# Kernel optimization log

Hardware: AMD Instinct MI355X
Metric: run time of the kernel (lower is better)

The kernel has to match this reference:

```python
import jax, jax.numpy as jnp
import numpy as np

MU = jnp.array([1.0, 0.9, 0.7, 0.5, 0.3, 0.1, -0.1, -0.3, -0.5, -0.7, -0.9], dtype=jnp.float32)
SIGMA = jnp.array([1e-3] + [0.1] * 10, dtype=jnp.float32)
H = 8  # n_head


def _lin(x, W, b):
    return x @ W.T + b


def _knrm_logsum(eq, ed, mq, md):
    # eq:[B,Q,D] ed:[B,L,D] mq:[B,Q] md:[B,L] -> [B,K]
    qn = eq / jnp.maximum(jnp.linalg.norm(eq, axis=2, keepdims=True), 1e-12)
    dn = ed / jnp.maximum(jnp.linalg.norm(ed, axis=2, keepdims=True), 1e-12)
    sim = jnp.einsum('bqe,bde->bqd', qn, dn)
    pv = jnp.exp(-(sim[..., None] - MU) ** 2 / (2.0 * SIGMA ** 2))  # [B,Q,L,K]
    ps = jnp.sum(pv * md[:, None, :, None], axis=2)                 # [B,Q,K]
    lps = jnp.log(jnp.clip(ps, 1e-10, None)) * mq[..., None] * 0.01
    return jnp.sum(lps, axis=1)


def _mha(x, Wq, bq, Wk, bk, Wv, bv, Wo, bo):
    # CyberZHG-style MultiHeadAttention: relu on q/k/v projections and output.
    B, L, D = x.shape
    dh = D // H

    def split(t):
        return t.reshape(B, L, H, dh).transpose(0, 2, 1, 3)

    q = split(jax.nn.relu(_lin(x, Wq, bq)))
    k = split(jax.nn.relu(_lin(x, Wk, bk)))
    v = split(jax.nn.relu(_lin(x, Wv, bv)))
    att = jax.nn.softmax(jnp.einsum('bhqe,bhke->bhqk', q, k) / jnp.sqrt(jnp.float32(dh)), axis=-1)
    y = jnp.einsum('bhqk,bhke->bhqe', att, v).transpose(0, 2, 1, 3).reshape(B, L, D)
    return jax.nn.relu(_lin(y, Wo, bo))


def _forward(masks_q, masks_d, masks_dcq, masks_dbody, emb, Wq, bq, Wk, bk, Wv, bv, Wo, bo,
             tW, tb, qdW, qdb, qbW, qbb, qcqW, qcqb, dcqW, dcqb, bcqW, bcqb,
             expW, expb, combW, combb, inputs_q, inputs_d, inputs_dcq, inputs_dbody):
    eq = emb[inputs_q]
    ed = emb[inputs_d]
    eb = emb[inputs_dbody]
    qd = jnp.tanh(_lin(_knrm_logsum(eq, ed, masks_q, masks_d), qdW, qdb))
    qb = jnp.tanh(_lin(_knrm_logsum(eq, eb, masks_q, masks_dbody), qbW, qbb))
    B, MN, ML = inputs_dcq.shape
    e_dcq = jax.nn.relu(_lin(emb[inputs_dcq.reshape(B, MN * ML)], tW, tb))
    enc_dcq = _mha(e_dcq, Wq, bq, Wk, bk, Wv, bv, Wo, bo).reshape(B, MN, ML, -1)
    enc_d = _mha(ed, Wq, bq, Wk, bk, Wv, bv, Wo, bo)
    enc_b = _mha(eb, Wq, bq, Wk, bk, Wv, bv, Wo, bo)

    def per_cq(i_dcq, m_dcq):  # i_dcq:[B,ML,D] m_dcq:[B,ML]
        return (_knrm_logsum(eq, i_dcq, masks_q, m_dcq),
                _knrm_logsum(enc_d, i_dcq, masks_d, m_dcq),
                _knrm_logsum(enc_b, i_dcq, masks_dbody, m_dcq))

    kq, kd, kb = jax.vmap(per_cq, in_axes=(1, 1))(enc_dcq, masks_dcq)  # [MN,B,K]
    qcqres = jnp.tanh(_lin(kq, qcqW, qcqb))      # [MN,B,1]
    qcqdattn = jnp.tanh(_lin(kd, dcqW, dcqb))
    qcqbattn = jnp.tanh(_lin(kb, bcqW, bcqb))
    qcqd = jnp.sum(qcqres * qcqdattn, axis=0)    # [B,1]
    qcqb2 = jnp.sum(qcqres * qcqbattn, axis=0)
    qcq = _lin(jnp.concatenate([qcqd, qcqb2], axis=1), expW, expb)
    return jnp.tanh(_lin(jnp.concatenate([qd, qb, qcq], axis=1), combW, combb)).squeeze()


def setup_inputs():
    B, Q, DL, BL, MN, ML, D, V = 32, 20, 64, 512, 8, 16, 128, 50000
    key = jax.random.key(0)
    ks = jax.random.split(key, 40)

    def w(i, shape, s=0.05):
        return jax.random.normal(ks[i], shape, jnp.float32) * s

    return {
        'inputs_q': jax.random.randint(ks[0], (B, Q), 1, V),
        'inputs_d': jax.random.randint(ks[1], (B, DL), 1, V),
        'inputs_dcq': jax.random.randint(ks[2], (B, MN, ML), 1, V),
        'inputs_dbody': jax.random.randint(ks[3], (B, BL), 1, V),
        'masks_q': jnp.ones((B, Q), jnp.float32),
        'masks_d': jnp.ones((B, DL), jnp.float32),
        'masks_dcq': jnp.ones((B, MN, ML), jnp.float32),
        'masks_dbody': jnp.ones((B, BL), jnp.float32),
        'emb': w(4, (V, D), 0.1).at[0].set(0.0),  # padding_idx=0
        'Wq': w(5, (D, D)), 'bq': w(6, (D,)),
        'Wk': w(7, (D, D)), 'bk': w(8, (D,)),
        'Wv': w(9, (D, D)), 'bv': w(10, (D,)),
        'Wo': w(11, (D, D)), 'bo': w(12, (D,)),
        'tW': w(13, (D, D)), 'tb': w(14, (D,)),
        'qdW': w(15, (1, 11)), 'qdb': w(16, (1,)),
        'qbW': w(17, (1, 11)), 'qbb': w(18, (1,)),
        'qcqW': w(19, (1, 11)), 'qcqb': w(20, (1,)),
        'dcqW': w(21, (1, 11)), 'dcqb': w(22, (1,)),
        'bcqW': w(23, (1, 11)), 'bcqb': w(24, (1,)),
        'expW': w(25, (1, 2)), 'expb': w(26, (1,)),
        'combW': w(27, (1, 3)), 'combb': w(28, (1,)),
    }


def reference(inputs_q, inputs_d, inputs_dcq, inputs_dbody, masks_q, masks_d, masks_dcq, masks_dbody,
              emb, Wq, bq, Wk, bk, Wv, bv, Wo, bo, tW, tb, qdW, qdb, qbW, qbb, qcqW, qcqb,
              dcqW, dcqb, bcqW, bcqb, expW, expb, combW, combb):
    return _forward(masks_q, masks_d, masks_dcq, masks_dbody, emb, Wq, bq, Wk, bk, Wv, bv, Wo, bo,
                    tW, tb, qdW, qdb, qbW, qbb, qcqW, qcqb, dcqW, dcqb, bcqW, bcqb,
                    expW, expb, combW, combb, inputs_q, inputs_d, inputs_dcq, inputs_dbody)
```

## Files before the change

kernel.cpp:

```cpp
#include <hip/hip_runtime.h>
#include <hip/hip_bf16.h>

#define BB 32
#define QL_ 20
#define DL_ 64
#define BL_ 512
#define MN_ 8
#define ML_ 16
#define DD 128
#define HH 8

#define ROWS_DCQ 4096
#define ROWS_D   2048
#define ROWS_B   16384
#define R_ALL    22528
#define ROWS_EQ  640
#define R_GATHER 23168

typedef float f2 __attribute__((ext_vector_type(2)));

__global__ __launch_bounds__(256) void gather_all(
    const int* __restrict__ in_q, const int* __restrict__ in_d,
    const int* __restrict__ in_dcq, const int* __restrict__ in_db,
    const float* __restrict__ emb, float* __restrict__ x_all, float* __restrict__ ytmp,
    float* __restrict__ inv_eq, float* __restrict__ inv_ed, float* __restrict__ inv_eb,
    float* __restrict__ zero_p, int nzero) {
    int blk = blockIdx.x;
    if (blk >= 2896) {
        int i = (blk - 2896) * 256 + threadIdx.x;
        if (i < nzero) zero_p[i] = 0.f;
        return;
    }
    int t = blk * 256 + threadIdx.x;
    int r = t >> 5, c = t & 31;
    const int* idx; float* outp; float* invp; int lr;
    if (r < ROWS_DCQ)              { idx = in_dcq; outp = ytmp + (size_t)r * DD;  invp = nullptr; lr = r; }
    else if (r < ROWS_DCQ + ROWS_D){ idx = in_d;   outp = x_all + (size_t)r * DD; invp = inv_ed;  lr = r - ROWS_DCQ; }
    else if (r < R_ALL)            { idx = in_db;  outp = x_all + (size_t)r * DD; invp = inv_eb;  lr = r - (ROWS_DCQ + ROWS_D); }
    else                           { idx = in_q;   outp = x_all + (size_t)r * DD; invp = inv_eq;  lr = r - R_ALL; }
    float4 val = ((const float4*)(emb + (size_t)idx[lr] * DD))[c];
    ((float4*)outp)[c] = val;
    float ss = val.x * val.x + val.y * val.y + val.z * val.z + val.w * val.w;
    ss += __shfl_xor(ss, 1, 64);
    ss += __shfl_xor(ss, 2, 64);
    ss += __shfl_xor(ss, 4, 64);
    ss += __shfl_xor(ss, 8, 64);
    ss += __shfl_xor(ss, 16, 64);
    if (c == 0 && invp) invp[lr] = 1.0f / fmaxf(sqrtf(ss), 1e-12f);
}

__device__ __forceinline__ void linear_body(float* __restrict__ wT, float* __restrict__ bs,
                                            const float* __restrict__ in, const float* __restrict__ W,
                                            const float* __restrict__ bias, float* __restrict__ out,
                                            float* __restrict__ inv_out, int block) {
    int t = threadIdx.x;
    for (int i = t; i < DD * DD; i += 256) {
        int o = i >> 7, e = i & 127;
        wT[e * 132 + o] = W[i];
    }
    if (t < 128) bs[t] = bias[t];
    __syncthreads();
    int og = t & 15, rg = t >> 4;
    int rowbase = block * 128 + rg * 8;
    f2 acc[8][4];
#pragma unroll
    for (int r = 0; r < 8; r++)
#pragma unroll
        for (int p = 0; p < 4; p++) acc[r][p] = f2{0.f, 0.f};
    for (int e4 = 0; e4 < 32; e4++) {
        float4 xv[8];
#pragma unroll
        for (int r = 0; r < 8; r++)
            xv[r] = *(const float4*)&in[(size_t)(rowbase + r) * DD + 4 * e4];
#pragma unroll
        for (int ee = 0; ee < 4; ee++) {
            int e = 4 * e4 + ee;
            float4 wa = *(const float4*)&wT[e * 132 + 8 * og];
            float4 wb = *(const float4*)&wT[e * 132 + 8 * og + 4];
            f2 w0 = {wa.x, wa.y}, w1 = {wa.z, wa.w}, w2 = {wb.x, wb.y}, w3 = {wb.z, wb.w};
#pragma unroll
            for (int r = 0; r < 8; r++) {
                float x = ((const float*)&xv[r])[ee];
                f2 x2 = {x, x};
                acc[r][0] = __builtin_elementwise_fma(x2, w0, acc[r][0]);
                acc[r][1] = __builtin_elementwise_fma(x2, w1, acc[r][1]);
                acc[r][2] = __builtin_elementwise_fma(x2, w2, acc[r][2]);
                acc[r][3] = __builtin_elementwise_fma(x2, w3, acc[r][3]);
            }
        }
    }
    float4 ba = *(const float4*)&bs[8 * og];
    float4 bbv = *(const float4*)&bs[8 * og + 4];
    float ss[8];
#pragma unroll
    for (int r = 0; r < 8; r++) {
        float o0 = fmaxf(acc[r][0].x + ba.x, 0.f);
        float o1 = fmaxf(acc[r][0].y + ba.y, 0.f);
        float o2 = fmaxf(acc[r][1].x + ba.z, 0.f);
        float o3 = fmaxf(acc[r][1].y + ba.w, 0.f);
        float o4 = fmaxf(acc[r][2].x + bbv.x, 0.f);
        float o5 = fmaxf(acc[r][2].y + bbv.y, 0.f);
        float o6 = fmaxf(acc[r][3].x + bbv.z, 0.f);
        float o7 = fmaxf(acc[r][3].y + bbv.w, 0.f);
        float4 s1 = {o0, o1, o2, o3}, s2 = {o4, o5, o6, o7};
        float* op = out + (size_t)(rowbase + r) * DD + 8 * og;
        *(float4*)op = s1;
        *(float4*)(op + 4) = s2;
        ss[r] = o0 * o0 + o1 * o1 + o2 * o2 + o3 * o3 + o4 * o4 + o5 * o5 + o6 * o6 + o7 * o7;
    }
    if (inv_out) {
#pragma unroll
        for (int r = 0; r < 8; r++) {
            ss[r] += __shfl_xor(ss[r], 1, 64);
            ss[r] += __shfl_xor(ss[r], 2, 64);
            ss[r] += __shfl_xor(ss[r], 4, 64);
            ss[r] += __shfl_xor(ss[r], 8, 64);
        }
#pragma unroll
        for (int r = 0; r < 8; r++)
            if (og == r) inv_out[rowbase + r] = 1.0f / fmaxf(sqrtf(ss[r]), 1e-12f);
    }
}

__global__ __launch_bounds__(256) void lin_kernel(const float* __restrict__ in, const float* __restrict__ W,
                                                  const float* __restrict__ bias, float* __restrict__ out,
                                                  float* __restrict__ inv_out) {
    __shared__ float wT[DD * 132];
    __shared__ float bs[DD];
    linear_body(wT, bs, in, W, bias, out, inv_out, blockIdx.x);
}

__global__ __launch_bounds__(256) void qkv_all(const float* __restrict__ x,
                                               const float* __restrict__ Wq, const float* __restrict__ bq,
                                               const float* __restrict__ Wk, const float* __restrict__ bk,
                                               const float* __restrict__ Wv, const float* __restrict__ bv,
                                               float* __restrict__ q, float* __restrict__ k, float* __restrict__ v) {
    __shared__ float wT[DD * 132];
    __shared__ float bs[DD];
    int sel = blockIdx.x / 176, blk = blockIdx.x % 176;
    const float* W = (sel == 0) ? Wq : (sel == 1) ? Wk : Wv;
    const float* B = (sel == 0) ? bq : (sel == 1) ? bk : bv;
    float* O = (sel == 0) ? q : (sel == 1) ? k : v;
    linear_body(wT, bs, x, W, B, O, nullptr, blk);
}

__device__ __forceinline__ void attn512_v6(float* __restrict__ sm,
                                           const float* __restrict__ q, const float* __restrict__ k,
                                           const float* __restrict__ v, float* __restrict__ y,
                                           int b, int h) {
    float* ks = sm;
    float* vs = sm + 512 * 16;
    int t = threadIdx.x;
    const size_t base = (size_t)b * 512 * DD + h * 16;
    for (int i = t; i < 512 * 4; i += 512) {
        int j = i >> 2, c = i & 3;
        *(float4*)&ks[j * 16 + 4 * c] = *(const float4*)&k[base + (size_t)j * DD + 4 * c];
        *(float4*)&vs[j * 16 + 4 * c] = *(const float4*)&v[base + (size_t)j * DD + 4 * c];
    }
    int w = t >> 6, lane = t & 63;
    int kg = w & 3, qw = w >> 2;
    int r0 = qw * 256 + lane;
    f2 qv[2][16];
#pragma unroll
    for (int p = 0; p < 2; p++) {
        const float* qa = q + base + (size_t)(r0 + p * 128) * DD;
        const float* qb2 = qa + 64 * DD;
#pragma unroll
        for (int c = 0; c < 4; c++) {
            float4 va = *(const float4*)(qa + 4 * c);
            float4 vb = *(const float4*)(qb2 + 4 * c);
            qv[p][4 * c + 0] = f2{va.x * 0.25f, vb.x * 0.25f};
            qv[p][4 * c + 1] = f2{va.y * 0.25f, vb.y * 0.25f};
            qv[p][4 * c + 2] = f2{va.z * 0.25f, vb.z * 0.25f};
            qv[p][4 * c + 3] = f2{va.w * 0.25f, vb.w * 0.25f};
        }
    }
    f2 acc[2][16];
    f2 l2[2] = {f2{0.f, 0.f}, f2{0.f, 0.f}};
#pragma unroll
    for (int p = 0; p < 2; p++)
#pragma unroll
        for (int e = 0; e < 16; e++) acc[p][e] = f2{0.f, 0.f};
    __syncthreads();
    int j0 = kg * 128;
    for (int j = j0; j < j0 + 128; j++) {
        float kk[16], vv[16];
#pragma unroll
        for (int c = 0; c < 4; c++) {
            *(float4*)&kk[4 * c] = *(const float4*)&ks[j * 16 + 4 * c];
            *(float4*)&vv[4 * c] = *(const float4*)&vs[j * 16 + 4 * c];
        }
        f2 d0a = qv[0][0] * f2{kk[0], kk[0]};
        f2 d1a = qv[0][1] * f2{kk[1], kk[1]};
        f2 d0b = qv[1][0] * f2{kk[0], kk[0]};
        f2 d1b = qv[1][1] * f2{kk[1], kk[1]};
#pragma unroll
        for (int e = 2; e < 16; e += 2) {
            d0a = __builtin_elementwise_fma(qv[0][e], f2{kk[e], kk[e]}, d0a);
            d1a = __builtin_elementwise_fma(qv[0][e + 1], f2{kk[e + 1], kk[e + 1]}, d1a);
            d0b = __builtin_elementwise_fma(qv[1][e], f2{kk[e], kk[e]}, d0b);
            d1b = __builtin_elementwise_fma(qv[1][e + 1], f2{kk[e + 1], kk[e + 1]}, d1b);
        }
        f2 da = d0a + d1a, db = d0b + d1b;
        f2 pa = {__expf(da.x), __expf(da.y)};
        f2 pb = {__expf(db.x), __expf(db.y)};
        l2[0] += pa;
        l2[1] += pb;
#pragma unroll
        for (int e = 0; e < 16; e++) {
            f2 ve = {vv[e], vv[e]};
            acc[0][e] = __builtin_elementwise_fma(pa, ve, acc[0][e]);
            acc[1][e] = __builtin_elementwise_fma(pb, ve, acc[1][e]);
        }
    }
    __syncthreads();
#pragma unroll
    for (int g = 1; g < 4; g++) {
        if (kg == g) {
#pragma unroll
            for (int p = 0; p < 2; p++) {
                int ra = r0 + p * 128;
                float* pa = &sm[ra * 20];
                float* pb = &sm[(ra + 64) * 20];
#pragma unroll
                for (int e = 0; e < 16; e++) { pa[e] = acc[p][e].x; pb[e] = acc[p][e].y; }
                pa[16] = l2[p].x;
                pb[16] = l2[p].y;
            }
        }
        __syncthreads();
        if (kg == 0) {
#pragma unroll
            for (int p = 0; p < 2; p++) {
                int ra = r0 + p * 128;
                const float* pa = &sm[ra * 20];
                const float* pb = &sm[(ra + 64) * 20];
#pragma unroll
                for (int e = 0; e < 16; e++) { acc[p][e].x += pa[e]; acc[p][e].y += pb[e]; }
                l2[p].x += pa[16];
                l2[p].y += pb[16];
            }
        }
        __syncthreads();
    }
    if (kg == 0) {
#pragma unroll
        for (int p = 0; p < 2; p++) {
            float ix = 1.0f / l2[p].x, iy = 1.0f / l2[p].y;
            float o0[16], o1[16];
#pragma unroll
            for (int e = 0; e < 16; e++) { o0[e] = acc[p][e].x * ix; o1[e] = acc[p][e].y * iy; }
            float* yp0 = y + base + (size_t)(r0 + p * 128) * DD;
            float* yp1 = yp0 + 64 * DD;
#pragma unroll
            for (int c = 0; c < 4; c++) {
                *(float4*)(yp0 + 4 * c) = *(const float4*)&o0[4 * c];
                *(float4*)(yp1 + 4 * c) = *(const float4*)&o1[4 * c];
            }
        }
    }
}

template <int L, int NQ>
__device__ __forceinline__ void attn_body(float* __restrict__ sm, const float* __restrict__ q,
                                          const float* __restrict__ k, const float* __restrict__ v,
                                          float* __restrict__ y, int b, int h) {
    constexpr int WAVES = 8;
    constexpr int WQ = L / (32 * NQ);
    constexpr int KG = WAVES / WQ;
    constexpr int KPG = L / KG;
    float* ks = sm;
    float* vs = sm + L * 16;
    int t = threadIdx.x;
    const size_t base = (size_t)b * L * DD + h * 16;
    for (int i = t; i < L * 4; i += 512) {
        int j = i >> 2, c = i & 3;
        *(float4*)&ks[j * 16 + 4 * c] = *(const float4*)&k[base + (size_t)j * DD + 4 * c];
        *(float4*)&vs[j * 16 + 4 * c] = *(const float4*)&v[base + (size_t)j * DD + 4 * c];
    }
    int w = t >> 6, lane = t & 63;
    int ls = lane & 31, eh = lane >> 5;
    int kg = w % KG, qw = w / KG;
    int qb2 = qw * 32 * NQ;
    f2 qv[NQ][4];
#pragma unroll
    for (int n = 0; n < NQ; n++) {
        int qr = qb2 + ls + 32 * n;
        const float* qp = q + base + (size_t)qr * DD + eh * 8;
        float4 a = *(const float4*)qp;
        float4 b4 = *(const float4*)(qp + 4);
        qv[n][0] = f2{a.x, a.y};   qv[n][1] = f2{a.z, a.w};
        qv[n][2] = f2{b4.x, b4.y}; qv[n][3] = f2{b4.z, b4.w};
    }
    f2 acc[NQ][4];
    float l[NQ];
#pragma unroll
    for (int n = 0; n < NQ; n++) {
#pragma unroll
        for (int m = 0; m < 4; m++) acc[n][m] = f2{0.f, 0.f};
        l[n] = 0.f;
    }
    __syncthreads();
    for (int j = kg * KPG; j < (kg + 1) * KPG; j++) {
        float4 ka = *(const float4*)&ks[j * 16 + eh * 8];
        float4 kb2 = *(const float4*)&ks[j * 16 + eh * 8 + 4];
        float4 va = *(const float4*)&vs[j * 16 + eh * 8];
        float4 vb2 = *(const float4*)&vs[j * 16 + eh * 8 + 4];
        f2 kk0 = {ka.x, ka.y}, kk1 = {ka.z, ka.w}, kk2 = {kb2.x, kb2.y}, kk3 = {kb2.z, kb2.w};
        f2 vv0 = {va.x, va.y}, vv1 = {va.z, va.w}, vv2 = {vb2.x, vb2.y}, vv3 = {vb2.z, vb2.w};
#pragma unroll
        for (int n = 0; n < NQ; n++) {
            f2 d2 = qv[n][0] * kk0;
            d2 = __builtin_elementwise_fma(qv[n][1], kk1, d2);
            d2 = __builtin_elementwise_fma(qv[n][2], kk2, d2);
            d2 = __builtin_elementwise_fma(qv[n][3], kk3, d2);
            float sh = d2.x + d2.y;
            float s = sh + __shfl_xor(sh, 32, 64);
            float p = __expf(s * 0.25f);
            l[n] += p;
            f2 p2 = {p, p};
            acc[n][0] = __builtin_elementwise_fma(p2, vv0, acc[n][0]);
            acc[n][1] = __builtin_elementwise_fma(p2, vv1, acc[n][1]);
            acc[n][2] = __builtin_elementwise_fma(p2, vv2, acc[n][2]);
            acc[n][3] = __builtin_elementwise_fma(p2, vv3, acc[n][3]);
        }
    }
    __syncthreads();
    if (kg > 0) {
#pragma unroll
        for (int n = 0; n < NQ; n++) {
            int qr = qb2 + ls + 32 * n;
            float* pp = &sm[((kg - 1) * L + qr) * 20 + eh * 10];
            *(f2*)&pp[0] = acc[n][0];
            *(f2*)&pp[2] = acc[n][1];
            *(f2*)&pp[4] = acc[n][2];
            *(f2*)&pp[6] = acc[n][3];
            pp[8] = l[n];
        }
    }
    __syncthreads();
    if (kg == 0) {
#pragma unroll
        for (int n = 0; n < NQ; n++) {
            int qr = qb2 + ls + 32 * n;
            f2 a0 = acc[n][0], a1 = acc[n][1], a2 = acc[n][2], a3 = acc[n][3];
            float lt = l[n];
#pragma unroll
            for (int g = 1; g < KG; g++) {
                const float* pp = &sm[((g - 1) * L + qr) * 20 + eh * 10];
                a0 += *(const f2*)&pp[0];
                a1 += *(const f2*)&pp[2];
                a2 += *(const f2*)&pp[4];
                a3 += *(const f2*)&pp[6];
                lt += pp[8];
            }
            float inv = 1.0f / lt;
            float4 o1 = {a0.x * inv, a0.y * inv, a1.x * inv, a1.y * inv};
            float4 o2 = {a2.x * inv, a2.y * inv, a3.x * inv, a3.y * inv};
            float* yp = y + base + (size_t)qr * DD + eh * 8;
            *(float4*)yp = o1;
            *(float4*)(yp + 4) = o2;
        }
    }
}

__global__ __launch_bounds__(512, 2) void attn_all(const float* __restrict__ qb_, const float* __restrict__ kb_,
                                                   const float* __restrict__ vb_, float* __restrict__ yb_) {
    __shared__ float sm[16384];
    int blk = blockIdx.x;
    if (blk < 256) {
        const size_t off = (size_t)(ROWS_DCQ + ROWS_D) * DD;
        attn512_v6(sm, qb_ + off, kb_ + off, vb_ + off, yb_ + off, blk & 31, blk >> 5);
    } else if (blk < 512) {
        int local = blk - 256;
        attn_body<128, 1>(sm, qb_, kb_, vb_, yb_, local & 31, local >> 5);
    } else {
        int local = blk - 512;
        const size_t off = (size_t)ROWS_DCQ * DD;
        attn_body<64, 1>(sm, qb_ + off, kb_ + off, vb_ + off, yb_ + off, local & 31, local >> 5);
    }
}

template <int QPT, int DPT>
__device__ void knrm_core(float* __restrict__ sm,
                          const float* __restrict__ Q, const float* __restrict__ invQ,
                          const float* __restrict__ mq, int QL, int q0, int qbase,
                          const float* __restrict__ D, const float* __restrict__ invD,
                          const float* __restrict__ md, int DL, int dbase, int mdbase,
                          float* __restrict__ out) {
    constexpr int QT = QPT * 16, DT = DPT * 16;
    float* qtile = sm;
    float* dtile = qtile + QT * 132;
    float* mdv = dtile + DT * 132;
    float* red = mdv + DT;
    float* outred = red + 4 * 16 * QPT * 11;
    const float MUc[11] = {1.0f, 0.9f, 0.7f, 0.5f, 0.3f, 0.1f, -0.1f, -0.3f, -0.5f, -0.7f, -0.9f};
    const float NC[11]  = {-500000.0f, -50.f, -50.f, -50.f, -50.f, -50.f, -50.f, -50.f, -50.f, -50.f, -50.f};
    int t = threadIdx.x;
    int tq = t & 15, td = t >> 4;
    if (t < 11) outred[t] = 0.f;
    for (int i = t; i < QT * 32; i += 256) {
        int r = i >> 5, c = i & 31;
        int qrow = q0 + r;
        float4 val = make_float4(0.f, 0.f, 0.f, 0.f);
        if (qrow < QL) {
            float s = invQ[qbase + qrow];
            float4 g = *(const float4*)(Q + (size_t)(qbase + qrow) * DD + 4 * c);
            val = make_float4(g.x * s, g.y * s, g.z * s, g.w * s);
        }
        *(float4*)&qtile[r * 132 + 4 * c] = val;
    }
    float ps[QPT][11];
#pragma unroll
    for (int i = 0; i < QPT; i++)
#pragma unroll
        for (int kk = 0; kk < 11; kk++) ps[i][kk] = 0.f;

    for (int d0 = 0; d0 < DL; d0 += DT) {
        for (int i = t; i < DT * 32; i += 256) {
            int r = i >> 5, c = i & 31;
            int drow = d0 + r;
            float4 val = make_float4(0.f, 0.f, 0.f, 0.f);
            if (drow < DL) {
                float s = invD[dbase + drow];
                float4 g = *(const float4*)(D + (size_t)(dbase + drow) * DD + 4 * c);
                val = make_float4(g.x * s, g.y * s, g.z * s, g.w * s);
            }
            *(float4*)&dtile[r * 132 + 4 * c] = val;
        }
        if (t < DT) mdv[t] = (d0 + t < DL) ? md[mdbase + d0 + t] : 0.f;
        __syncthreads();
        float dot[QPT][DPT];
#pragma unroll
        for (int i = 0; i < QPT; i++)
#pragma unroll
            for (int j = 0; j < DPT; j++) dot[i][j] = 0.f;
#pragma unroll 2
        for (int e4 = 0; e4 < 32; e4++) {
            float4 qv[QPT], dv[DPT];
#pragma unroll
            for (int i = 0; i < QPT; i++) qv[i] = *(const float4*)&qtile[(tq + 16 * i) * 132 + 4 * e4];
#pragma unroll
            for (int j = 0; j < DPT; j++) dv[j] = *(const float4*)&dtile[(td + 16 * j) * 132 + 4 * e4];
#pragma unroll
            for (int i = 0; i < QPT; i++)
#pragma unroll
                for (int j = 0; j < DPT; j++)
                    dot[i][j] += qv[i].x * dv[j].x + qv[i].y * dv[j].y + qv[i].z * dv[j].z + qv[i].w * dv[j].w;
        }
#pragma unroll
        for (int j = 0; j < DPT; j++) {
            float m = mdv[td + 16 * j];
#pragma unroll
            for (int i = 0; i < QPT; i++) {
                float sim = dot[i][j];
#pragma unroll
                for (int kk = 0; kk < 11; kk++) {
                    float df = sim - MUc[kk];
                    ps[i][kk] = fmaf(__expf(df * df * NC[kk]), m, ps[i][kk]);
                }
            }
        }
        __syncthreads();
    }
#pragma unroll
    for (int i = 0; i < QPT; i++)
#pragma unroll
        for (int kk = 0; kk < 11; kk++) {
            ps[i][kk] += __shfl_xor(ps[i][kk], 16, 64);
            ps[i][kk] += __shfl_xor(ps[i][kk], 32, 64);
        }
    int w = t >> 6;
    if ((t & 63) < 16) {
#pragma unroll
        for (int i = 0; i < QPT; i++)
#pragma unroll
            for (int kk = 0; kk < 11; kk++) red[(w * 16 + tq) * (QPT * 11) + i * 11 + kk] = ps[i][kk];
    }
    __syncthreads();
    for (int i = t; i < 16 * QPT * 11; i += 256) {
        int tq2 = i / (QPT * 11);
        int rem = i - tq2 * (QPT * 11);
        int qi = rem / 11, kk = rem - qi * 11;
        float s = red[(0 * 16 + tq2) * (QPT * 11) + qi * 11 + kk] + red[(1 * 16 + tq2) * (QPT * 11) + qi * 11 + kk]
                + red[(2 * 16 + tq2) * (QPT * 11) + qi * 11 + kk] + red[(3 * 16 + tq2) * (QPT * 11) + qi * 11 + kk];
        int qrow = q0 + tq2 + 16 * qi;
        if (qrow < QL) {
            float lps = logf(fmaxf(s, 1e-10f)) * mq[qbase + qrow] * 0.01f;
            atomicAdd(&outred[kk], lps);
        }
    }
    __syncthreads();
    if (t < 11) atomicAdd(&out[t], outred[t]);
}

__global__ __launch_bounds__(256) void knrm_all(
    const float* __restrict__ eq, const float* __restrict__ inv_eq, const float* __restrict__ mask_q,
    const float* __restrict__ ed, const float* __restrict__ inv_ed, const float* __restrict__ mask_d,
    const float* __restrict__ eb, const float* __restrict__ inv_eb, const float* __restrict__ mask_db,
    const float* __restrict__ enc_d, const float* __restrict__ inv_encd,
    const float* __restrict__ enc_b, const float* __restrict__ inv_encb,
    const float* __restrict__ enc_dcq, const float* __restrict__ inv_encdcq, const float* __restrict__ mask_dcq,
    float* __restrict__ qdk, float* __restrict__ qbk,
    float* __restrict__ kq, float* __restrict__ kd, float* __restrict__ kb) {
    __shared__ float sm[14155];
    int blk = blockIdx.x;
    if (blk < 32) {
        int b = blk;
        knrm_core<2, 4>(sm, eq, inv_eq, mask_q, QL_, 0, b * QL_, ed, inv_ed, mask_d, DL_, b * DL_, b * DL_, qdk + b * 11);
    } else if (blk < 64) {
        int b = blk - 32;
        knrm_core<2, 4>(sm, eq, inv_eq, mask_q, QL_, 0, b * QL_, eb, inv_eb, mask_db, BL_, b * BL_, b * BL_, qbk + b * 11);
    } else {
        int u = blk - 64;
        int sub = u % 10;
        int ib = u / 10;
        int b = ib & 31, inst = ib >> 5;
        int dbase = b * (MN_ * ML_) + inst * ML_;
        if (sub == 0)
            knrm_core<4, 1>(sm, eq, inv_eq, mask_q, QL_, 0, b * QL_, enc_dcq, inv_encdcq, mask_dcq, ML_, dbase, dbase,
                            kq + (size_t)(inst * BB + b) * 11);
        else if (sub == 1)
            knrm_core<4, 1>(sm, enc_d, inv_encd, mask_d, DL_, 0, b * DL_, enc_dcq, inv_encdcq, mask_dcq, ML_, dbase, dbase,
                            kd + (size_t)(inst * BB + b) * 11);
        else
            knrm_core<4, 1>(sm, enc_b, inv_encb, mask_db, BL_, (sub - 2) * 64, b * BL_, enc_dcq, inv_encdcq, mask_dcq, ML_,
                            dbase, dbase, kb + (size_t)(inst * BB + b) * 11);
    }
}

__device__ inline float dot11(const float* w, const float* x) {
    float s = 0.f;
#pragma unroll
    for (int k = 0; k < 11; k++) s += w[k] * x[k];
    return s;
}

__global__ void final_kernel(const float* __restrict__ qdk, const float* __restrict__ qbk,
                             const float* __restrict__ kq, const float* __restrict__ kd,
                             const float* __restrict__ kb,
                             const float* qdW, const float* qdb, const float* qbW, const float* qbb,
                             const float* qcqW, const float* qcqb, const float* dcqW, const float* dcqb,
                             const float* bcqW, const float* bcqb, const float* expW, const float* expb,
                             const float* combW, const float* combb, float* __restrict__ out) {
    int b = threadIdx.x;
    if (b >= BB) return;
    float qd = tanhf(dot11(qdW, qdk + b * 11) + qdb[0]);
    float qb = tanhf(dot11(qbW, qbk + b * 11) + qbb[0]);
    float qcqd = 0.f, qcqb2 = 0.f;
    for (int i = 0; i < MN_; i++) {
        int base = (i * BB + b) * 11;
        float r  = tanhf(dot11(qcqW, kq + base) + qcqb[0]);
        float da = tanhf(dot11(dcqW, kd + base) + dcqb[0]);
        float ba = tanhf(dot11(bcqW, kb + base) + bcqb[0]);
        qcqd += r * da;
        qcqb2 += r * ba;
    }
    float qcq = expW[0] * qcqd + expW[1] * qcqb2 + expb[0];
    out[b] = tanhf(combW[0] * qd + combW[1] * qb + combW[2] * qcq + combb[0]);
}

extern "C" void kernel_launch(void* const* d_in, const int* in_sizes, int n_in,
                              void* d_out, int out_size, void* d_ws, size_t ws_size,
                              hipStream_t stream) {
    const int*   in_q    = (const int*)d_in[0];
    const int*   in_d    = (const int*)d_in[1];
    const int*   in_dcq  = (const int*)d_in[2];
    const int*   in_db   = (const int*)d_in[3];
    const float* mask_q  = (const float*)d_in[4];
    const float* mask_d  = (const float*)d_in[5];
    const float* mask_dcq= (const float*)d_in[6];
    const float* mask_db = (const float*)d_in[7];
    const float* emb     = (const float*)d_in[8];
    const float* Wq = (const float*)d_in[9];   const float* bq = (const float*)d_in[10];
    const float* Wk = (const float*)d_in[11];  const float* bk = (const float*)d_in[12];
    const float* Wv = (const float*)d_in[13];  const float* bv = (const float*)d_in[14];
    const float* Wo = (const float*)d_in[15];  const float* bo = (const float*)d_in[16];
    const float* tW = (const float*)d_in[17];  const float* tb = (const float*)d_in[18];
    const float* qdW = (const float*)d_in[19]; const float* qdb = (const float*)d_in[20];
    const float* qbW = (const float*)d_in[21]; const float* qbb = (const float*)d_in[22];
    const float* qcqW = (const float*)d_in[23];const float* qcqb = (const float*)d_in[24];
    const float* dcqW = (const float*)d_in[25];const float* dcqb = (const float*)d_in[26];
    const float* bcqW = (const float*)d_in[27];const float* bcqb = (const float*)d_in[28];
    const float* expW = (const float*)d_in[29];const float* expb = (const float*)d_in[30];
    const float* combW = (const float*)d_in[31];const float* combb = (const float*)d_in[32];
    float* out = (float*)d_out;

    float* ws = (float*)d_ws;
    size_t off = 0;
    auto alloc = [&](size_t n) { float* p = ws + off; off += n; return p; };
    float* x_all = alloc((size_t)R_GATHER * DD);
    float* qbuf  = alloc((size_t)R_ALL * DD);
    float* kbuf  = alloc((size_t)R_ALL * DD);
    float* vbuf  = alloc((size_t)R_ALL * DD);
    float* inv_eq  = alloc(ROWS_EQ);
    float* inv_ed  = alloc(ROWS_D);
    float* inv_eb  = alloc(ROWS_B);
    float* inv_enc = alloc(R_ALL);
    float* qdk = alloc(BB * 11);
    float* qbk = alloc(BB * 11);
    float* kq  = alloc(MN_ * BB * 11);
    float* kd  = alloc(MN_ * BB * 11);
    float* kb  = alloc(MN_ * BB * 11);
    (void)ws_size; (void)in_sizes; (void)n_in; (void)out_size;

    const float* eq      = x_all + (size_t)R_ALL * DD;
    const float* ed      = x_all + (size_t)ROWS_DCQ * DD;
    const float* eb      = x_all + (size_t)(ROWS_DCQ + ROWS_D) * DD;
    float* enc_all = kbuf;
    const float* enc_dcq = enc_all;
    const float* enc_d   = enc_all + (size_t)ROWS_DCQ * DD;
    const float* enc_b   = enc_all + (size_t)(ROWS_DCQ + ROWS_D) * DD;
    const float* inv_encdcq = inv_enc;
    const float* inv_encd   = inv_enc + ROWS_DCQ;
    const float* inv_encb   = inv_enc + ROWS_DCQ + ROWS_D;

    gather_all<<<2932, 256, 0, stream>>>(in_q, in_d, in_dcq, in_db, emb,
                                         x_all, kbuf, inv_eq, inv_ed, inv_eb, qdk, 9152);
    lin_kernel<<<ROWS_DCQ / 128, 256, 0, stream>>>(kbuf, tW, tb, x_all, nullptr);
    qkv_all<<<3 * (R_ALL / 128), 256, 0, stream>>>(x_all, Wq, bq, Wk, bk, Wv, bv, qbuf, kbuf, vbuf);
    attn_all<<<768, 512, 0, stream>>>(qbuf, kbuf, vbuf, qbuf);
    lin_kernel<<<R_ALL / 128, 256, 0, stream>>>(qbuf, Wo, bo, enc_all, inv_enc);
    knrm_all<<<2624, 256, 0, stream>>>(eq, inv_eq, mask_q, ed, inv_ed, mask_d, eb, inv_eb, mask_db,
                                       enc_d, inv_encd, enc_b, inv_encb, enc_dcq, inv_encdcq, mask_dcq,
                                       qdk, qbk, kq, kd, kb);
    final_kernel<<<1, 64, 0, stream>>>(qdk, qbk, kq, kd, kb,
                                       qdW, qdb, qbW, qbb, qcqW, qcqb, dcqW, dcqb,
                                       bcqW, bcqb, expW, expb, combW, combb, out);
}
```

Before: 375.8 us.

## Split attention and KNRM work into smaller blocks with more parallelism

Attention blocks shrink from 512 to 256 threads, and the 512-length attention now splits its queries across two blocks. V is read directly from global memory instead of being staged in LDS, which halves shared memory per block and allows more resident blocks. The q-body KNRM is split into 16 document chunks that atomically accumulate raw kernel sums per query, and the final kernel now applies the log and mask. The dcq KNRM work is also split more finely. This raises block count and occupancy at the cost of more global V traffic, more atomics and redundant K loads.

```diff
diff --git a/kernel.cpp b/kernel.cpp
--- a/kernel.cpp
+++ b/kernel.cpp
@@ -144,22 +144,19 @@
     linear_body(wT, bs, x, W, B, O, nullptr, blk);
 }
 
-__device__ __forceinline__ void attn512_v6(float* __restrict__ sm,
+__device__ __forceinline__ void attn512_v7(float* __restrict__ sm,
                                            const float* __restrict__ q, const float* __restrict__ k,
                                            const float* __restrict__ v, float* __restrict__ y,
-                                           int b, int h) {
+                                           int b, int h, int qh) {
     float* ks = sm;
-    float* vs = sm + 512 * 16;
     int t = threadIdx.x;
     const size_t base = (size_t)b * 512 * DD + h * 16;
-    for (int i = t; i < 512 * 4; i += 512) {
+    for (int i = t; i < 512 * 4; i += 256) {
         int j = i >> 2, c = i & 3;
         *(float4*)&ks[j * 16 + 4 * c] = *(const float4*)&k[base + (size_t)j * DD + 4 * c];
-        *(float4*)&vs[j * 16 + 4 * c] = *(const float4*)&v[base + (size_t)j * DD + 4 * c];
-    }
-    int w = t >> 6, lane = t & 63;
-    int kg = w & 3, qw = w >> 2;
-    int r0 = qw * 256 + lane;
+    }
+    int kg = t >> 6, lane = t & 63;
+    int r0 = qh * 256 + lane;
     f2 qv[2][16];
 #pragma unroll
     for (int p = 0; p < 2; p++) {
@@ -184,11 +181,12 @@
     __syncthreads();
     int j0 = kg * 128;
     for (int j = j0; j < j0 + 128; j++) {
+        const float* vp = v + base + (size_t)j * DD;
         float kk[16], vv[16];
 #pragma unroll
         for (int c = 0; c < 4; c++) {
             *(float4*)&kk[4 * c] = *(const float4*)&ks[j * 16 + 4 * c];
-            *(float4*)&vv[4 * c] = *(const float4*)&vs[j * 16 + 4 * c];
+            *(float4*)&vv[4 * c] = *(const float4*)(vp + 4 * c);
         }
         f2 d0a = qv[0][0] * f2{kk[0], kk[0]};
         f2 d1a = qv[0][1] * f2{kk[1], kk[1]};
@@ -219,9 +217,9 @@
         if (kg == g) {
 #pragma unroll
             for (int p = 0; p < 2; p++) {
-                int ra = r0 + p * 128;
-                float* pa = &sm[ra * 20];
-                float* pb = &sm[(ra + 64) * 20];
+                int lr = lane + p * 128;
+                float* pa = &sm[lr * 17];
+                float* pb = &sm[(lr + 64) * 17];
 #pragma unroll
                 for (int e = 0; e < 16; e++) { pa[e] = acc[p][e].x; pb[e] = acc[p][e].y; }
                 pa[16] = l2[p].x;
@@ -232,9 +230,9 @@
         if (kg == 0) {
 #pragma unroll
             for (int p = 0; p < 2; p++) {
-                int ra = r0 + p * 128;
-                const float* pa = &sm[ra * 20];
-                const float* pb = &sm[(ra + 64) * 20];
+                int lr = lane + p * 128;
+                const float* pa = &sm[lr * 17];
+                const float* pb = &sm[(lr + 64) * 17];
 #pragma unroll
                 for (int e = 0; e < 16; e++) { acc[p][e].x += pa[e]; acc[p][e].y += pb[e]; }
                 l2[p].x += pa[16];
@@ -265,18 +263,16 @@
 __device__ __forceinline__ void attn_body(float* __restrict__ sm, const float* __restrict__ q,
                                           const float* __restrict__ k, const float* __restrict__ v,
                                           float* __restrict__ y, int b, int h) {
-    constexpr int WAVES = 8;
+    constexpr int WAVES = 4;
     constexpr int WQ = L / (32 * NQ);
     constexpr int KG = WAVES / WQ;
     constexpr int KPG = L / KG;
     float* ks = sm;
-    float* vs = sm + L * 16;
     int t = threadIdx.x;
     const size_t base = (size_t)b * L * DD + h * 16;
-    for (int i = t; i < L * 4; i += 512) {
+    for (int i = t; i < L * 4; i += 256) {
         int j = i >> 2, c = i & 3;
         *(float4*)&ks[j * 16 + 4 * c] = *(const float4*)&k[base + (size_t)j * DD + 4 * c];
-        *(float4*)&vs[j * 16 + 4 * c] = *(const float4*)&v[base + (size_t)j * DD + 4 * c];
     }
     int w = t >> 6, lane = t & 63;
     int ls = lane & 31, eh = lane >> 5;
@@ -302,10 +298,11 @@
     }
     __syncthreads();
     for (int j = kg * KPG; j < (kg + 1) * KPG; j++) {
+        const float* vp = v + base + (size_t)j * DD + eh * 8;
         float4 ka = *(const float4*)&ks[j * 16 + eh * 8];
         float4 kb2 = *(const float4*)&ks[j * 16 + eh * 8 + 4];
-        float4 va = *(const float4*)&vs[j * 16 + eh * 8];
-        float4 vb2 = *(const float4*)&vs[j * 16 + eh * 8 + 4];
+        float4 va = *(const float4*)vp;
+        float4 vb2 = *(const float4*)(vp + 4);
         f2 kk0 = {ka.x, ka.y}, kk1 = {ka.z, ka.w}, kk2 = {kb2.x, kb2.y}, kk3 = {kb2.z, kb2.w};
         f2 vv0 = {va.x, va.y}, vv1 = {va.z, va.w}, vv2 = {vb2.x, vb2.y}, vv3 = {vb2.z, vb2.w};
 #pragma unroll
@@ -326,7 +323,7 @@
         }
     }
     __syncthreads();
-    if (kg > 0) {
+    if (KG > 1 && kg > 0) {
 #pragma unroll
         for (int n = 0; n < NQ; n++) {
             int qr = qb2 + ls + 32 * n;
@@ -364,24 +361,25 @@
     }
 }
 
-__global__ __launch_bounds__(512, 2) void attn_all(const float* __restrict__ qb_, const float* __restrict__ kb_,
+__global__ __launch_bounds__(256, 4) void attn_all(const float* __restrict__ qb_, const float* __restrict__ kb_,
                                                    const float* __restrict__ vb_, float* __restrict__ yb_) {
-    __shared__ float sm[16384];
+    __shared__ float sm[8192];
     int blk = blockIdx.x;
-    if (blk < 256) {
+    if (blk < 512) {
         const size_t off = (size_t)(ROWS_DCQ + ROWS_D) * DD;
-        attn512_v6(sm, qb_ + off, kb_ + off, vb_ + off, yb_ + off, blk & 31, blk >> 5);
-    } else if (blk < 512) {
-        int local = blk - 256;
+        int qh = blk >> 8, local = blk & 255;
+        attn512_v7(sm, qb_ + off, kb_ + off, vb_ + off, yb_ + off, local & 31, local >> 5, qh);
+    } else if (blk < 768) {
+        int local = blk - 512;
         attn_body<128, 1>(sm, qb_, kb_, vb_, yb_, local & 31, local >> 5);
     } else {
-        int local = blk - 512;
+        int local = blk - 768;
         const size_t off = (size_t)ROWS_DCQ * DD;
         attn_body<64, 1>(sm, qb_ + off, kb_ + off, vb_ + off, yb_ + off, local & 31, local >> 5);
     }
 }
 
-template <int QPT, int DPT>
+template <int QPT, int DPT, bool RAW>
 __device__ void knrm_core(float* __restrict__ sm,
                           const float* __restrict__ Q, const float* __restrict__ invQ,
                           const float* __restrict__ mq, int QL, int q0, int qbase,
@@ -398,7 +396,7 @@
     const float NC[11]  = {-500000.0f, -50.f, -50.f, -50.f, -50.f, -50.f, -50.f, -50.f, -50.f, -50.f, -50.f};
     int t = threadIdx.x;
     int tq = t & 15, td = t >> 4;
-    if (t < 11) outred[t] = 0.f;
+    if (!RAW && t < 11) outred[t] = 0.f;
     for (int i = t; i < QT * 32; i += 256) {
         int r = i >> 5, c = i & 31;
         int qrow = q0 + r;
@@ -486,12 +484,18 @@
                 + red[(2 * 16 + tq2) * (QPT * 11) + qi * 11 + kk] + red[(3 * 16 + tq2) * (QPT * 11) + qi * 11 + kk];
         int qrow = q0 + tq2 + 16 * qi;
         if (qrow < QL) {
-            float lps = logf(fmaxf(s, 1e-10f)) * mq[qbase + qrow] * 0.01f;
-            atomicAdd(&outred[kk], lps);
-        }
-    }
-    __syncthreads();
-    if (t < 11) atomicAdd(&out[t], outred[t]);
+            if (RAW) {
+                atomicAdd(&out[qrow * 11 + kk], s);
+            } else {
+                float lps = logf(fmaxf(s, 1e-10f)) * mq[qbase + qrow] * 0.01f;
+                atomicAdd(&outred[kk], lps);
+            }
+        }
+    }
+    if (!RAW) {
+        __syncthreads();
+        if (t < 11) atomicAdd(&out[t], outred[t]);
+    }
 }
 
 __global__ __launch_bounds__(256) void knrm_all(
@@ -501,31 +505,37 @@
     const float* __restrict__ enc_d, const float* __restrict__ inv_encd,
     const float* __restrict__ enc_b, const float* __restrict__ inv_encb,
     const float* __restrict__ enc_dcq, const float* __restrict__ inv_encdcq, const float* __restrict__ mask_dcq,
-    float* __restrict__ qdk, float* __restrict__ qbk,
+    float* __restrict__ qdk, float* __restrict__ ps_qb,
     float* __restrict__ kq, float* __restrict__ kd, float* __restrict__ kb) {
-    __shared__ float sm[14155];
+    __shared__ float sm[9920];
     int blk = blockIdx.x;
     if (blk < 32) {
         int b = blk;
-        knrm_core<2, 4>(sm, eq, inv_eq, mask_q, QL_, 0, b * QL_, ed, inv_ed, mask_d, DL_, b * DL_, b * DL_, qdk + b * 11);
-    } else if (blk < 64) {
-        int b = blk - 32;
-        knrm_core<2, 4>(sm, eq, inv_eq, mask_q, QL_, 0, b * QL_, eb, inv_eb, mask_db, BL_, b * BL_, b * BL_, qbk + b * 11);
+        knrm_core<2, 2, false>(sm, eq, inv_eq, mask_q, QL_, 0, b * QL_,
+                               ed, inv_ed, mask_d, DL_, b * DL_, b * DL_, qdk + b * 11);
+    } else if (blk < 544) {
+        int u = blk - 32;
+        int b = u & 31, ch = u >> 5;
+        knrm_core<2, 2, true>(sm, eq, inv_eq, mask_q, QL_, 0, b * QL_,
+                              eb, inv_eb, mask_db, 32, b * BL_ + ch * 32, b * BL_ + ch * 32,
+                              ps_qb + b * (QL_ * 11));
     } else {
-        int u = blk - 64;
-        int sub = u % 10;
-        int ib = u / 10;
-        int b = ib & 31, inst = ib >> 5;
+        int u = blk - 544;
+        int g = u / 19, sub = u % 19;
+        int b = g & 31, inst = g >> 5;
         int dbase = b * (MN_ * ML_) + inst * ML_;
         if (sub == 0)
-            knrm_core<4, 1>(sm, eq, inv_eq, mask_q, QL_, 0, b * QL_, enc_dcq, inv_encdcq, mask_dcq, ML_, dbase, dbase,
-                            kq + (size_t)(inst * BB + b) * 11);
-        else if (sub == 1)
-            knrm_core<4, 1>(sm, enc_d, inv_encd, mask_d, DL_, 0, b * DL_, enc_dcq, inv_encdcq, mask_dcq, ML_, dbase, dbase,
-                            kd + (size_t)(inst * BB + b) * 11);
+            knrm_core<2, 1, false>(sm, eq, inv_eq, mask_q, QL_, 0, b * QL_,
+                                   enc_dcq, inv_encdcq, mask_dcq, ML_, dbase, dbase,
+                                   kq + (size_t)(inst * BB + b) * 11);
+        else if (sub < 3)
+            knrm_core<2, 1, false>(sm, enc_d, inv_encd, mask_d, DL_, (sub - 1) * 32, b * DL_,
+                                   enc_dcq, inv_encdcq, mask_dcq, ML_, dbase, dbase,
+                                   kd + (size_t)(inst * BB + b) * 11);
         else
-            knrm_core<4, 1>(sm, enc_b, inv_encb, mask_db, BL_, (sub - 2) * 64, b * BL_, enc_dcq, inv_encdcq, mask_dcq, ML_,
-                            dbase, dbase, kb + (size_t)(inst * BB + b) * 11);
+            knrm_core<2, 1, false>(sm, enc_b, inv_encb, mask_db, BL_, (sub - 3) * 32, b * BL_,
+                                   enc_dcq, inv_encdcq, mask_dcq, ML_, dbase, dbase,
+                                   kb + (size_t)(inst * BB + b) * 11);
     }
 }
 
@@ -536,17 +546,27 @@
     return s;
 }
 
-__global__ void final_kernel(const float* __restrict__ qdk, const float* __restrict__ qbk,
-                             const float* __restrict__ kq, const float* __restrict__ kd,
-                             const float* __restrict__ kb,
-                             const float* qdW, const float* qdb, const float* qbW, const float* qbb,
-                             const float* qcqW, const float* qcqb, const float* dcqW, const float* dcqb,
-                             const float* bcqW, const float* bcqb, const float* expW, const float* expb,
-                             const float* combW, const float* combb, float* __restrict__ out) {
-    int b = threadIdx.x;
+__global__ __launch_bounds__(384) void final_kernel(
+    const float* __restrict__ qdk, const float* __restrict__ ps_qb, const float* __restrict__ mask_q,
+    const float* __restrict__ kq, const float* __restrict__ kd, const float* __restrict__ kb,
+    const float* qdW, const float* qdb, const float* qbW, const float* qbb,
+    const float* qcqW, const float* qcqb, const float* dcqW, const float* dcqb,
+    const float* bcqW, const float* bcqb, const float* expW, const float* expb,
+    const float* combW, const float* combb, float* __restrict__ out) {
+    __shared__ float qbk_s[BB * 11];
+    int t = threadIdx.x;
+    if (t < BB * 11) {
+        int b = t / 11, kk = t % 11;
+        float s = 0.f;
+        for (int qq = 0; qq < QL_; qq++)
+            s += logf(fmaxf(ps_qb[b * (QL_ * 11) + qq * 11 + kk], 1e-10f)) * mask_q[b * QL_ + qq];
+        qbk_s[t] = s * 0.01f;
+    }
+    __syncthreads();
+    int b = t;
     if (b >= BB) return;
     float qd = tanhf(dot11(qdW, qdk + b * 11) + qdb[0]);
-    float qb = tanhf(dot11(qbW, qbk + b * 11) + qbb[0]);
+    float qb = tanhf(dot11(qbW, qbk_s + b * 11) + qbb[0]);
     float qcqd = 0.f, qcqb2 = 0.f;
     for (int i = 0; i < MN_; i++) {
         int base = (i * BB + b) * 11;
@@ -597,12 +617,13 @@
     float* inv_ed  = alloc(ROWS_D);
     float* inv_eb  = alloc(ROWS_B);
     float* inv_enc = alloc(R_ALL);
-    float* qdk = alloc(BB * 11);
-    float* qbk = alloc(BB * 11);
-    float* kq  = alloc(MN_ * BB * 11);
-    float* kd  = alloc(MN_ * BB * 11);
-    float* kb  = alloc(MN_ * BB * 11);
+    float* qdk   = alloc(BB * 11);
+    float* kq    = alloc(MN_ * BB * 11);
+    float* kd    = alloc(MN_ * BB * 11);
+    float* kb    = alloc(MN_ * BB * 11);
+    float* ps_qb = alloc(BB * QL_ * 11);
     (void)ws_size; (void)in_sizes; (void)n_in; (void)out_size;
+    const int kZeroCount = BB * 11 + 3 * MN_ * BB * 11 + BB * QL_ * 11;
 
     const float* eq      = x_all + (size_t)R_ALL * DD;
     const float* ed      = x_all + (size_t)ROWS_DCQ * DD;
@@ -615,16 +636,17 @@
     const float* inv_encd   = inv_enc + ROWS_DCQ;
     const float* inv_encb   = inv_enc + ROWS_DCQ + ROWS_D;
 
-    gather_all<<<2932, 256, 0, stream>>>(in_q, in_d, in_dcq, in_db, emb,
-                                         x_all, kbuf, inv_eq, inv_ed, inv_eb, qdk, 9152);
+    gather_all<<<2896 + (kZeroCount + 255) / 256, 256, 0, stream>>>(in_q, in_d, in_dcq, in_db, emb,
+                                                                    x_all, kbuf, inv_eq, inv_ed, inv_eb,
+                                                                    qdk, kZeroCount);
     lin_kernel<<<ROWS_DCQ / 128, 256, 0, stream>>>(kbuf, tW, tb, x_all, nullptr);
     qkv_all<<<3 * (R_ALL / 128), 256, 0, stream>>>(x_all, Wq, bq, Wk, bk, Wv, bv, qbuf, kbuf, vbuf);
-    attn_all<<<768, 512, 0, stream>>>(qbuf, kbuf, vbuf, qbuf);
+    attn_all<<<1024, 256, 0, stream>>>(qbuf, kbuf, vbuf, qbuf);
     lin_kernel<<<R_ALL / 128, 256, 0, stream>>>(qbuf, Wo, bo, enc_all, inv_enc);
-    knrm_all<<<2624, 256, 0, stream>>>(eq, inv_eq, mask_q, ed, inv_ed, mask_d, eb, inv_eb, mask_db,
+    knrm_all<<<5408, 256, 0, stream>>>(eq, inv_eq, mask_q, ed, inv_ed, mask_d, eb, inv_eb, mask_db,
                                        enc_d, inv_encd, enc_b, inv_encb, enc_dcq, inv_encdcq, mask_dcq,
-                                       qdk, qbk, kq, kd, kb);
-    final_kernel<<<1, 64, 0, stream>>>(qdk, qbk, kq, kd, kb,
-                                       qdW, qdb, qbW, qbb, qcqW, qcqb, dcqW, dcqb,
-                                       bcqW, bcqb, expW, expb, combW, combb, out);
-}
+                                       qdk, ps_qb, kq, kd, kb);
+    final_kernel<<<1, 384, 0, stream>>>(qdk, ps_qb, mask_q, kq, kd, kb,
+                                        qdW, qdb, qbW, qbb, qcqW, qcqb, dcqW, dcqb,
+                                        bcqW, bcqb, expW, expb, combW, combb, out);
+}
```

Result: slower. 562.8 us (+49.8%).
